# Performance work log

Measured on AMD Instinct MI355X. Metric: run time of the kernel, lower is better.

Reference implementation:

```python
import jax, jax.numpy as jnp
import numpy as np
from jax import lax

PRE_NMS_TOPN = 6000
POST_NMS_TOPN = 300
NMS_IOU = 0.7
VARIANCES = np.array([0.1, 0.1, 0.2, 0.2], dtype=np.float32)


def setup_inputs() -> dict:
    key = jax.random.key(0)
    k1, k2, k3, k4 = jax.random.split(key, 4)
    B, FH, FW, K = 32, 128, 128, 9
    A = FH * FW * K  # 147456 total anchors
    rpn_bbox_deltas = jax.random.normal(k1, (B, A, 4), dtype=jnp.float32) * 0.1
    rpn_labels = jax.random.normal(k2, (B, FH, FW, K), dtype=jnp.float32)
    # Anchors in [y1, x1, y2, x2] with y1<y2, x1<x2 on a ~1024px image.
    ctr = jax.random.uniform(k3, (A, 2), dtype=jnp.float32) * 1024.0
    wh = jax.random.uniform(k4, (A, 2), dtype=jnp.float32) * 224.0 + 32.0
    anchors = jnp.concatenate([ctr - 0.5 * wh, ctr + 0.5 * wh], axis=-1)
    return {"rpn_bbox_deltas": rpn_bbox_deltas, "rpn_labels": rpn_labels, "anchors": anchors}


def get_bboxes_from_deltas(anchors, deltas):
    # anchors: [A, 4] (y1,x1,y2,x2); deltas: [B, A, 4] (dy,dx,dh,dw)
    anc_w = anchors[..., 3] - anchors[..., 1]
    anc_h = anchors[..., 2] - anchors[..., 0]
    anc_cx = anchors[..., 1] + 0.5 * anc_w
    anc_cy = anchors[..., 0] + 0.5 * anc_h
    bb_w = jnp.exp(deltas[..., 3]) * anc_w
    bb_h = jnp.exp(deltas[..., 2]) * anc_h
    bb_cx = deltas[..., 1] * anc_w + anc_cx
    bb_cy = deltas[..., 0] * anc_h + anc_cy
    y1 = bb_cy - 0.5 * bb_h
    x1 = bb_cx - 0.5 * bb_w
    y2 = bb_h + y1
    x2 = bb_w + x1
    return jnp.stack([y1, x1, y2, x2], axis=-1)


def nms_per_image(boxes, scores, iou_threshold, num_keep):
    # boxes: [N, 4] sorted by descending score; scores: [N]
    y1, x1, y2, x2 = boxes[:, 0], boxes[:, 1], boxes[:, 2], boxes[:, 3]
    areas = (y2 - y1) * (x2 - x1)

    def step(scores_rem, _):
        idx = jnp.argmax(scores_rem)
        valid = jnp.isfinite(scores_rem[idx])
        b = boxes[idx]
        iy1 = jnp.maximum(b[0], y1)
        ix1 = jnp.maximum(b[1], x1)
        iy2 = jnp.minimum(b[2], y2)
        ix2 = jnp.minimum(b[3], x2)
        inter = jnp.clip(iy2 - iy1, 0.0) * jnp.clip(ix2 - ix1, 0.0)
        b_area = (b[2] - b[0]) * (b[3] - b[1])
        iou = inter / (areas + b_area - inter + 1e-9)
        # IoU(box, itself) == 1 > threshold, so the picked box is also suppressed.
        new_scores = jnp.where(iou > iou_threshold, -jnp.inf, scores_rem)
        return new_scores, (idx, valid)

    _, (keep_idx, valid) = lax.scan(step, scores, None, length=num_keep)
    vf = valid.astype(boxes.dtype)
    keep_boxes = boxes[keep_idx] * vf[:, None]  # zero-pad invalid slots
    keep_scores = scores[keep_idx] * vf
    return keep_boxes, keep_scores


def reference(rpn_bbox_deltas, rpn_labels, anchors):
    A = anchors.shape[0]
    B = rpn_bbox_deltas.shape[0]
    deltas = rpn_bbox_deltas.reshape(B, A, 4) * jnp.asarray(VARIANCES)
    labels = jax.nn.softmax(rpn_labels, axis=-1).reshape(B, A)
    rpn_bboxes = get_bboxes_from_deltas(anchors, deltas)  # [B, A, 4]
    # top-k pre-NMS filter (lax.top_k output is already sorted descending)
    pre_scores, pre_idx = lax.top_k(labels, PRE_NMS_TOPN)  # [B, P]
    pre_boxes = jnp.take_along_axis(rpn_bboxes, pre_idx[..., None], axis=1)  # [B, P, 4]
    nms_fn = lambda b, s: nms_per_image(b, s, NMS_IOU, POST_NMS_TOPN)
    roi_bboxes, roi_scores = jax.vmap(nms_fn)(pre_boxes, pre_scores)
    return roi_bboxes, roi_scores
```

## Files before the change

kernel.cpp:

```cpp
#include <hip/hip_runtime.h>
#include <cstdint>
#include <cstddef>

#pragma clang fp contract(off)

#define KCLS 9
#define PRE_N 6000
#define POST_N 300
#define NMS_IOU_T 0.7f
#define HIST_BLOCK 256
#define CHUNKS_PER_IMG 32
#define NMS_BLOCK 512
#define PICK_BLOCK 256
#define NSEG 8
#define SEG_CAP 2048
#define RANK_LDS 8192

#define SUPP(pb, pa, mbx, mar, out) \
    bool out; { \
        float iy1_ = fmaxf((pb).x, (mbx).x); \
        float ix1_ = fmaxf((pb).y, (mbx).y); \
        float iy2_ = fminf((pb).z, (mbx).z); \
        float ix2_ = fminf((pb).w, (mbx).w); \
        float ih_ = iy2_ - iy1_; ih_ = ih_ > 0.f ? ih_ : 0.f; \
        float iw_ = ix2_ - ix1_; iw_ = iw_ > 0.f ? iw_ : 0.f; \
        float inter_ = ih_ * iw_; \
        float den_ = (mar) + (pa) - inter_ + 1e-9f; \
        float hi_ = 0.7000007f * den_; \
        float lo_ = 0.6999993f * den_; \
        out = inter_ > hi_; \
        if (inter_ >= lo_ && inter_ <= hi_) out = (inter_ / den_) > NMS_IOU_T; \
    }

__global__ void __launch_bounds__(256)
softmax_hist_kernel(const float* __restrict__ labels,
                    float* __restrict__ scores,
                    unsigned int* __restrict__ ghist,
                    int gpi) {
    __shared__ float buf[256 * KCLS];
    __shared__ unsigned int h[2048];
    const int tid = threadIdx.x;
    for (int i = tid; i < 2048; i += 256) h[i] = 0u;

    const size_t gbase = (size_t)blockIdx.x * (256 * KCLS);
    const float4* lin4 = (const float4*)(labels + gbase);
    float4* b4 = (float4*)buf;
    for (int i = tid; i < 576; i += 256) b4[i] = lin4[i];
    __syncthreads();

    float v[KCLS];
    float m = -1e30f;
    #pragma unroll
    for (int k = 0; k < KCLS; ++k) { v[k] = buf[tid * KCLS + k]; m = fmaxf(m, v[k]); }
    float e[KCLS];
    float s = 0.f;
    #pragma unroll
    for (int k = 0; k < KCLS; ++k) { e[k] = expf(v[k] - m); s += e[k]; }
    #pragma unroll
    for (int k = 0; k < KCLS; ++k) {
        float r = e[k] / s;
        buf[tid * KCLS + k] = r;
        atomicAdd(&h[(__float_as_uint(r) >> 21) & 2047u], 1u);
    }
    __syncthreads();

    float4* o4 = (float4*)(scores + gbase);
    for (int i = tid; i < 576; i += 256) o4[i] = b4[i];

    const int img0 = (blockIdx.x * 256) / gpi;
    unsigned int* gh = ghist + (size_t)img0 * 2048;
    for (int i = tid; i < 2048; i += 256) {
        unsigned int c = h[i];
        if (c) atomicAdd(&gh[i], c);
    }
}

__global__ void hist_kernel(const float* __restrict__ scores,
                            unsigned int* __restrict__ ghist,
                            const unsigned int* __restrict__ state,
                            int A, int shift, int bins, unsigned int pmask) {
    __shared__ unsigned int h[2048];
    const int img = blockIdx.y;
    const int chunk = blockIdx.x;
    const int tid = threadIdx.x;
    for (int i = tid; i < bins; i += HIST_BLOCK) h[i] = 0u;
    __syncthreads();
    unsigned int prefix = state[img * 2 + 0] & pmask;
    const int per = A / CHUNKS_PER_IMG;
    const float* sc = scores + (size_t)img * A + (size_t)chunk * per;
    for (int i = tid; i < per; i += HIST_BLOCK) {
        unsigned int v = __float_as_uint(sc[i]);
        if ((v & pmask) == prefix)
            atomicAdd(&h[(v >> shift) & (unsigned)(bins - 1)], 1u);
    }
    __syncthreads();
    unsigned int* gh = ghist + (size_t)img * 2048;
    for (int i = tid; i < bins; i += HIST_BLOCK) {
        unsigned int c = h[i];
        if (c) atomicAdd(&gh[i], c);
    }
}

__global__ void __launch_bounds__(PICK_BLOCK)
pick_kernel(const unsigned int* __restrict__ ghist,
            unsigned int* __restrict__ state,
            int shift, int bins, int first_pass) {
    const int img = blockIdx.x;
    const int t = threadIdx.x;
    const unsigned int* gh = ghist + (size_t)img * 2048;
    __shared__ unsigned int cnt[2048];
    __shared__ unsigned int ssum[PICK_BLOCK];
    const int per = bins / PICK_BLOCK;
    unsigned int my = 0;
    for (int i = 0; i < per; ++i) {
        unsigned int c = gh[t * per + i];
        cnt[t * per + i] = c;
        my += c;
    }
    ssum[t] = my;
    __syncthreads();
    for (int d = 1; d < PICK_BLOCK; d <<= 1) {
        unsigned int v = (t + d < PICK_BLOCK) ? ssum[t + d] : 0u;
        __syncthreads();
        ssum[t] += v;
        __syncthreads();
    }
    unsigned int prefix = first_pass ? 0u : state[img * 2 + 0];
    unsigned int krem = first_pass ? (unsigned)PRE_N : state[img * 2 + 1];
    unsigned int above = ssum[t] - my;
    if (above < krem && ssum[t] >= krem) {
        unsigned int cum = above;
        for (int b = per - 1; b >= 0; --b) {
            unsigned int c = cnt[t * per + b];
            if (cum + c >= krem) {
                state[img * 2 + 0] = prefix | ((unsigned int)(t * per + b) << shift);
                state[img * 2 + 1] = krem - cum;
                break;
            }
            cum += c;
        }
    }
}

#define CE(a, b, u) { if ((v[a] > v[b]) == (u)) { unsigned long long t_ = v[a]; v[a] = v[b]; v[b] = t_; } }
#define REG3(u) { CE(0,4,u) CE(1,5,u) CE(2,6,u) CE(3,7,u) \
                  CE(0,2,u) CE(1,3,u) CE(4,6,u) CE(5,7,u) \
                  CE(0,1,u) CE(2,3,u) CE(4,5,u) CE(6,7,u) }

__global__ void __launch_bounds__(512)
compact_sort_kernel(const float* __restrict__ scores,
                    const unsigned int* __restrict__ state,
                    unsigned long long* __restrict__ pool,
                    unsigned int* __restrict__ counts,
                    int A) {
    __shared__ unsigned long long lin[SEG_CAP];
    __shared__ unsigned int plo[2][SEG_CAP];
    __shared__ unsigned int phi[2][SEG_CAP];
    __shared__ unsigned int cnt;
    const int img = blockIdx.y;
    const int seg = blockIdx.x;
    const int tid = threadIdx.x;
    const int lane = tid & 63;
    const int w = tid >> 6;
    const float* sc = scores + (size_t)img * A;
    const unsigned int T = state[img * 2 + 0];

    if (tid == 0) cnt = 0u;
    for (int i = tid; i < SEG_CAP; i += 512) lin[i] = ~0ull;
    __syncthreads();

    const int ngr = A >> 6;
    const int nj = ngr / NSEG;
    for (int j = w; j < nj; j += 8) {
        int g = seg + j * NSEG;
        int i = (g << 6) + lane;
        unsigned int sv = __float_as_uint(sc[i]);
        bool push = (sv >= T);
        unsigned long long bal = __ballot(push ? 1 : 0);
        if (push) {
            int leader = __ffsll(bal) - 1;
            int rank = __popcll(bal & ((1ull << lane) - 1ull));
            unsigned int base = 0;
            if (lane == leader) base = atomicAdd(&cnt, (unsigned int)__popcll(bal));
            base = (unsigned int)__shfl((int)base, leader);
            unsigned int pos = base + (unsigned int)rank;
            if (pos < SEG_CAP)
                lin[pos] = (((unsigned long long)(~sv)) << 32) | (unsigned long long)(unsigned int)i;
        }
    }
    __syncthreads();

    int n = (int)cnt; if (n > SEG_CAP) n = SEG_CAP;
    int P2 = 512; while (P2 < n) P2 <<= 1;
    const int NT = P2 >> 3;
    const int t = tid;
    const bool act = (t < NT);

    unsigned long long v[8];
    if (act) {
        #pragma unroll
        for (int e = 0; e < 8; ++e) v[e] = lin[(t << 3) + e];
        CE(0,1,true) CE(2,3,false) CE(4,5,true) CE(6,7,false)
        CE(0,2,true) CE(1,3,true) CE(4,6,false) CE(5,7,false)
        CE(0,1,true) CE(2,3,true) CE(4,5,false) CE(6,7,false)
        bool u8 = ((t & 1) == 0);
        REG3(u8)
    }
    int b = 0;
    for (int k = 16; k <= P2; k <<= 1) {
        const bool up = (((t << 3) & k) == 0);
        for (int j = k >> 1; j >= 8; j >>= 1) {
            const int c = j >> 3;
            if (act) {
                #pragma unroll
                for (int e = 0; e < 8; ++e) {
                    int idx = e * NT + t;
                    plo[b][idx] = (unsigned int)v[e];
                    phi[b][idx] = (unsigned int)(v[e] >> 32);
                }
            }
            __syncthreads();
            if (act) {
                const int q = t ^ c;
                const bool keep_min = (up == ((t & c) == 0));
                #pragma unroll
                for (int e = 0; e < 8; ++e) {
                    int idx = e * NT + q;
                    unsigned long long wv = ((unsigned long long)phi[b][idx] << 32)
                                          | (unsigned long long)plo[b][idx];
                    bool less = v[e] < wv;
                    v[e] = (less == keep_min) ? v[e] : wv;
                }
            }
            b ^= 1;
        }
        if (act) { REG3(up) }
    }

    unsigned long long* gp = pool + ((size_t)img * NSEG + seg) * SEG_CAP;
    if (act) {
        #pragma unroll
        for (int e = 0; e < 8; ++e) {
            int r = (t << 3) + e;
            if (r < n) gp[r] = v[e];
        }
    }
    if (tid == 0) counts[img * NSEG + seg] = (unsigned int)n;
}

__global__ void __launch_bounds__(256)
rank_decode_kernel(const unsigned long long* __restrict__ pool,
                   const unsigned int* __restrict__ counts,
                   const float* __restrict__ deltas,
                   const float* __restrict__ anchors,
                   float* __restrict__ pre_boxes,
                   float* __restrict__ pre_scores,
                   int A) {
    __shared__ unsigned long long arr[RANK_LDS];
    const int img = blockIdx.y;
    const int seg = blockIdx.x;
    const int tid = threadIdx.x;

    int c[NSEG], off[NSEG + 1];
    const unsigned long long* gp[NSEG];
    off[0] = 0;
    #pragma unroll
    for (int s = 0; s < NSEG; ++s) {
        int cs = (int)counts[img * NSEG + s];
        if (cs > SEG_CAP) cs = SEG_CAP;
        c[s] = cs;
        off[s + 1] = off[s] + cs;
        gp[s] = pool + ((size_t)img * NSEG + s) * SEG_CAP;
    }
    const int total = off[NSEG];
    const bool inlds = (total <= RANK_LDS);
    if (inlds) {
        #pragma unroll
        for (int s = 0; s < NSEG; ++s)
            for (int i = tid; i < c[s]; i += 256) arr[off[s] + i] = gp[s][i];
    }
    __syncthreads();

    const int m = c[seg];
    for (int i = tid; i < m; i += 256) {
        unsigned long long key = inlds ? arr[off[seg] + i] : gp[seg][i];
        int pos = i;
        #pragma unroll
        for (int s = 0; s < NSEG; ++s) {
            if (s == seg) continue;
            const unsigned long long* base = inlds ? (arr + off[s]) : gp[s];
            int lo = 0, hi = c[s];
            while (lo < hi) {
                int mid = (lo + hi) >> 1;
                if (base[mid] < key) lo = mid + 1; else hi = mid;
            }
            pos += lo;
        }
        if (pos < PRE_N) {
            unsigned int bidx = (unsigned int)(key & 0xFFFFFFFFull);
            unsigned int sbits = ~((unsigned int)(key >> 32));
            float score = __uint_as_float(sbits);
            float a0 = anchors[(size_t)bidx * 4 + 0];
            float a1 = anchors[(size_t)bidx * 4 + 1];
            float a2 = anchors[(size_t)bidx * 4 + 2];
            float a3 = anchors[(size_t)bidx * 4 + 3];
            const float* dd = deltas + ((size_t)img * A + bidx) * 4;
            float d0 = dd[0] * 0.1f;
            float d1 = dd[1] * 0.1f;
            float d2 = dd[2] * 0.2f;
            float d3 = dd[3] * 0.2f;
            float anc_w = a3 - a1;
            float anc_h = a2 - a0;
            float anc_cx = a1 + 0.5f * anc_w;
            float anc_cy = a0 + 0.5f * anc_h;
            float bb_w = expf(d3) * anc_w;
            float bb_h = expf(d2) * anc_h;
            float bb_cx = d1 * anc_w + anc_cx;
            float bb_cy = d0 * anc_h + anc_cy;
            float y1 = bb_cy - 0.5f * bb_h;
            float x1 = bb_cx - 0.5f * bb_w;
            float y2 = bb_h + y1;
            float x2 = bb_w + x1;
            float* ob = pre_boxes + ((size_t)img * PRE_N + pos) * 4;
            ob[0] = y1; ob[1] = x1; ob[2] = y2; ob[3] = x2;
            pre_scores[(size_t)img * PRE_N + pos] = score;
        }
    }
}

__global__ void __launch_bounds__(NMS_BLOCK)
nms_kernel(const float* __restrict__ pre_boxes,
           const float* __restrict__ pre_scores,
           float* __restrict__ out_boxes,
           float* __restrict__ out_scores) {
    const int img = blockIdx.x;
    const int tid = threadIdx.x;
    const int lane = tid & 63;
    const int grp = tid >> 6;
    const float4* bb4 = (const float4*)(pre_boxes + (size_t)img * PRE_N * 4);

    __shared__ float4 kept[POST_N];
    __shared__ float  kept_area[POST_N];
    __shared__ int    kept_idx[POST_N];
    __shared__ float4 chunkbox[64];
    __shared__ unsigned long long part[8][64];
    __shared__ unsigned long long supcol[64];
    __shared__ unsigned long long chunk_alive;
    __shared__ int kept_cnt;

    if (tid == 0) kept_cnt = 0;

    const int NCH = (PRE_N + 63) >> 6;

    float4 nb = make_float4(0.f, 0.f, 0.f, 0.f);
    if (grp == 0) nb = bb4[lane];

    for (int c = 0; c < NCH; ++c) {
        const int base = c << 6;
        if (grp == 0) chunkbox[lane] = nb;
        if (tid == 0) {
            int rem = PRE_N - base;
            chunk_alive = (rem >= 64) ? ~0ull : ((1ull << rem) - 1ull);
        }
        __syncthreads();

        if (grp == 0 && c + 1 < NCH) {
            int j = base + 64 + lane;
            nb = (j < PRE_N) ? bb4[j] : make_float4(0.f, 0.f, 0.f, 0.f);
        }

        const int K = kept_cnt;
        float4 mb = chunkbox[lane];
        float marea = (mb.z - mb.x) * (mb.w - mb.y);

        bool sup = false;
        for (int k = grp; k < K; k += 8) {
            float4 pb = kept[k];
            float pa = kept_area[k];
            SUPP(pb, pa, mb, marea, s)
            if (s) { sup = true; break; }
        }
        unsigned long long bal = __ballot(sup ? 1 : 0);
        if (lane == 0 && bal) atomicAnd(&chunk_alive, ~bal);

        unsigned long long pm = 0ull;
        #pragma unroll
        for (int u = 0; u < 8; ++u) {
            const int i = (grp << 3) + u;
            float4 pb = chunkbox[i];
            float pa = (pb.z - pb.x) * (pb.w - pb.y);
            SUPP(pb, pa, mb, marea, s)
            if (s) pm |= (1ull << i);
        }
        part[grp][lane] = pm;
        __syncthreads();

        if (grp == 0) {
            unsigned long long col = part[0][lane] | part[1][lane] | part[2][lane] | part[3][lane]
                                   | part[4][lane] | part[5][lane] | part[6][lane] | part[7][lane];
            supcol[lane] = col;
            const unsigned long long extm = chunk_alive;
            unsigned long long aliveset = 0ull;
            int kc = K;
            #pragma unroll 8
            for (int i = 0; i < 64; ++i) {
                unsigned long long mi = supcol[i];
                bool keep = (((extm >> i) & 1ull) != 0ull) &&
                            ((mi & aliveset) == 0ull) && (kc < POST_N);
                if (keep) {
                    if (lane == i) {
                        kept[kc] = mb;
                        kept_area[kc] = marea;
                        kept_idx[kc] = base + i;
                    }
                    aliveset |= (1ull << i);
                    ++kc;
                }
            }
            if (lane == 0) kept_cnt = kc;
        }
        __syncthreads();
        if (kept_cnt >= POST_N) break;
    }

    const int kc = kept_cnt;
    for (int r = tid; r < kc; r += NMS_BLOCK) {
        float4 bx = kept[r];
        float* ob = out_boxes + ((size_t)img * POST_N + r) * 4;
        ob[0] = bx.x; ob[1] = bx.y; ob[2] = bx.z; ob[3] = bx.w;
        out_scores[(size_t)img * POST_N + r] =
            pre_scores[(size_t)img * PRE_N + kept_idx[r]];
    }
}

extern "C" void kernel_launch(void* const* d_in, const int* in_sizes, int n_in,
                              void* d_out, int out_size, void* d_ws, size_t ws_size,
                              hipStream_t stream) {
    const float* deltas  = (const float*)d_in[0];
    const float* labels  = (const float*)d_in[1];
    const float* anchors = (const float*)d_in[2];
    float* out = (float*)d_out;

    const int A = in_sizes[2] / 4;
    const int B = in_sizes[0] / (A * 4);
    const int ngroups = in_sizes[1] / KCLS;
    const int gpi = ngroups / B;

    float* scores     = (float*)d_ws;
    float* pre_boxes  = scores + (size_t)B * A;
    float* pre_scores = pre_boxes + (size_t)B * PRE_N * 4;
    unsigned int* hist  = (unsigned int*)(pre_scores + (size_t)B * PRE_N);
    unsigned int* state = hist + (size_t)2 * B * 2048;
    unsigned long long* pool = (unsigned long long*)(state + (size_t)B * 2);
    unsigned int* counts = (unsigned int*)(pool + (size_t)B * NSEG * SEG_CAP);

    float* out_boxes  = out;
    float* out_scores = out + (size_t)B * POST_N * 4;

    hipMemsetAsync(d_out, 0, (size_t)out_size * sizeof(float), stream);
    hipMemsetAsync(hist, 0, ((size_t)2 * B * 2048 + 2 * B) * sizeof(unsigned int), stream);

    softmax_hist_kernel<<<ngroups / 256, 256, 0, stream>>>(
        labels, scores, hist + (size_t)0 * B * 2048, gpi);
    pick_kernel<<<B, PICK_BLOCK, 0, stream>>>(hist + (size_t)0 * B * 2048, state, 21, 2048, 1);

    dim3 hgrid(CHUNKS_PER_IMG, B);
    hist_kernel<<<hgrid, HIST_BLOCK, 0, stream>>>(
        scores, hist + (size_t)1 * B * 2048, state, A, 10, 2048, 0xFFE00000u);
    pick_kernel<<<B, PICK_BLOCK, 0, stream>>>(hist + (size_t)1 * B * 2048, state, 10, 2048, 0);

    dim3 sgrid(NSEG, B);
    compact_sort_kernel<<<sgrid, 512, 0, stream>>>(scores, state, pool, counts, A);
    rank_decode_kernel<<<sgrid, 256, 0, stream>>>(pool, counts, deltas, anchors,
                                                  pre_boxes, pre_scores, A);

    nms_kernel<<<B, NMS_BLOCK, 0, stream>>>(pre_boxes, pre_scores, out_boxes, out_scores);
}
```

Before: 260.9 us.

## Process 128-box chunks in NMS with 1024 threads and bitmask-driven serial pick

The NMS kernel now takes 128 candidate boxes per iteration with 1024 threads, where each of the 16 waves covers one half-chunk and one slot of the kept-box stride. Intra-chunk suppression rows are built with ballots into lo/hi bitmasks. The serial keep loop walks alive bits with ffs and shuffles instead of scanning all 64 entries. The next chunk is double-buffered in LDS so it can be written before the barrier. The aim is to halve the number of block-wide barrier rounds and shorten the serial resolve step, at the cost of more wasted IoU work once the kept list saturates mid-chunk.

```diff
diff --git a/kernel.cpp b/kernel.cpp
--- a/kernel.cpp
+++ b/kernel.cpp
@@ -10,11 +10,11 @@
 #define NMS_IOU_T 0.7f
 #define HIST_BLOCK 256
 #define CHUNKS_PER_IMG 32
-#define NMS_BLOCK 512
 #define PICK_BLOCK 256
 #define NSEG 8
 #define SEG_CAP 2048
 #define RANK_LDS 8192
+#define CHUNK2 128
 
 #define SUPP(pb, pa, mbx, mar, out) \
     bool out; { \
@@ -328,7 +328,7 @@
     }
 }
 
-__global__ void __launch_bounds__(NMS_BLOCK)
+__global__ void __launch_bounds__(1024)
 nms_kernel(const float* __restrict__ pre_boxes,
            const float* __restrict__ pre_scores,
            float* __restrict__ out_boxes,
@@ -337,85 +337,102 @@
     const int tid = threadIdx.x;
     const int lane = tid & 63;
     const int grp = tid >> 6;
+    const int half = grp & 1;
+    const int kslot = grp >> 1;
     const float4* bb4 = (const float4*)(pre_boxes + (size_t)img * PRE_N * 4);
 
     __shared__ float4 kept[POST_N];
     __shared__ float  kept_area[POST_N];
     __shared__ int    kept_idx[POST_N];
-    __shared__ float4 chunkbox[64];
-    __shared__ unsigned long long part[8][64];
-    __shared__ unsigned long long supcol[64];
-    __shared__ unsigned long long chunk_alive;
+    __shared__ float4 chunkbox[2][CHUNK2];
+    __shared__ unsigned long long rows_lo[CHUNK2];
+    __shared__ unsigned long long rows_hi[CHUNK2];
+    __shared__ unsigned long long alive_lo[2], alive_hi[2];
     __shared__ int kept_cnt;
 
-    if (tid == 0) kept_cnt = 0;
-
-    const int NCH = (PRE_N + 63) >> 6;
+    const int NPAIR = (PRE_N + CHUNK2 - 1) / CHUNK2;
 
     float4 nb = make_float4(0.f, 0.f, 0.f, 0.f);
-    if (grp == 0) nb = bb4[lane];
-
-    for (int c = 0; c < NCH; ++c) {
-        const int base = c << 6;
-        if (grp == 0) chunkbox[lane] = nb;
-        if (tid == 0) {
-            int rem = PRE_N - base;
-            chunk_alive = (rem >= 64) ? ~0ull : ((1ull << rem) - 1ull);
-        }
-        __syncthreads();
-
-        if (grp == 0 && c + 1 < NCH) {
-            int j = base + 64 + lane;
-            nb = (j < PRE_N) ? bb4[j] : make_float4(0.f, 0.f, 0.f, 0.f);
-        }
-
+    if (tid < CHUNK2) {
+        chunkbox[0][tid] = bb4[tid];
+        int j = CHUNK2 + tid;
+        nb = (j < PRE_N) ? bb4[j] : make_float4(0.f, 0.f, 0.f, 0.f);
+    }
+    if (tid == 0) { alive_lo[0] = ~0ull; alive_hi[0] = ~0ull; kept_cnt = 0; }
+    __syncthreads();
+
+    for (int p = 0; p < NPAIR; ++p) {
+        const int base = p * CHUNK2;
+        const int cur = p & 1;
         const int K = kept_cnt;
-        float4 mb = chunkbox[lane];
+        const int mybox = (half << 6) + lane;
+        float4 mb = chunkbox[cur][mybox];
         float marea = (mb.z - mb.x) * (mb.w - mb.y);
 
         bool sup = false;
-        for (int k = grp; k < K; k += 8) {
+        for (int k = kslot; k < K; k += 8) {
             float4 pb = kept[k];
             float pa = kept_area[k];
             SUPP(pb, pa, mb, marea, s)
             if (s) { sup = true; break; }
         }
         unsigned long long bal = __ballot(sup ? 1 : 0);
-        if (lane == 0 && bal) atomicAnd(&chunk_alive, ~bal);
-
-        unsigned long long pm = 0ull;
-        #pragma unroll
-        for (int u = 0; u < 8; ++u) {
-            const int i = (grp << 3) + u;
-            float4 pb = chunkbox[i];
+        if (lane == 0 && bal) {
+            if (half == 0) atomicAnd(&alive_lo[cur], ~bal);
+            else           atomicAnd(&alive_hi[cur], ~bal);
+        }
+
+        #pragma unroll 4
+        for (int u = 0; u < 16; ++u) {
+            const int i = (kslot << 4) + u;
+            float4 pb = chunkbox[cur][i];
             float pa = (pb.z - pb.x) * (pb.w - pb.y);
             SUPP(pb, pa, mb, marea, s)
-            if (s) pm |= (1ull << i);
-        }
-        part[grp][lane] = pm;
+            unsigned long long rb = __ballot(s ? 1 : 0);
+            if (lane == 0) {
+                if (half == 0) rows_lo[i] = rb; else rows_hi[i] = rb;
+            }
+        }
+
+        if (tid < CHUNK2) {
+            chunkbox[cur ^ 1][tid] = nb;
+            int j = base + 2 * CHUNK2 + tid;
+            nb = (j < PRE_N) ? bb4[j] : make_float4(0.f, 0.f, 0.f, 0.f);
+        }
+        if (tid == 0) {
+            int rem = PRE_N - (base + CHUNK2);
+            if (rem > 0) {
+                alive_lo[cur ^ 1] = (rem >= 64) ? ~0ull : ((1ull << rem) - 1ull);
+                int rh = rem - 64;
+                alive_hi[cur ^ 1] = (rh >= 64) ? ~0ull : ((rh > 0) ? ((1ull << rh) - 1ull) : 0ull);
+            }
+        }
         __syncthreads();
 
         if (grp == 0) {
-            unsigned long long col = part[0][lane] | part[1][lane] | part[2][lane] | part[3][lane]
-                                   | part[4][lane] | part[5][lane] | part[6][lane] | part[7][lane];
-            supcol[lane] = col;
-            const unsigned long long extm = chunk_alive;
-            unsigned long long aliveset = 0ull;
+            unsigned long long myA_lo = rows_lo[lane];
+            unsigned long long myA_hi = rows_hi[lane];
+            unsigned long long myB_lo = rows_lo[64 + lane];
+            unsigned long long myB_hi = rows_hi[64 + lane];
+            unsigned long long rlo = alive_lo[cur];
+            unsigned long long rhi = alive_hi[cur];
             int kc = K;
-            #pragma unroll 8
-            for (int i = 0; i < 64; ++i) {
-                unsigned long long mi = supcol[i];
-                bool keep = (((extm >> i) & 1ull) != 0ull) &&
-                            ((mi & aliveset) == 0ull) && (kc < POST_N);
-                if (keep) {
-                    if (lane == i) {
-                        kept[kc] = mb;
-                        kept_area[kc] = marea;
-                        kept_idx[kc] = base + i;
-                    }
-                    aliveset |= (1ull << i);
-                    ++kc;
+            while ((rlo | rhi) && kc < POST_N) {
+                const bool lo = (rlo != 0ull);
+                const int i = lo ? (__ffsll(rlo) - 1) : (64 + __ffsll(rhi) - 1);
+                if (lane == 0) {
+                    float4 kb = chunkbox[cur][i];
+                    kept[kc] = kb;
+                    kept_area[kc] = (kb.z - kb.x) * (kb.w - kb.y);
+                    kept_idx[kc] = base + i;
                 }
+                const int src = i & 63;
+                unsigned long long r_lo = __shfl(lo ? myA_lo : myB_lo, src);
+                unsigned long long r_hi = __shfl(lo ? myA_hi : myB_hi, src);
+                if (lo) rlo &= ~(1ull << i); else rhi &= ~(1ull << (i - 64));
+                rlo &= ~r_lo;
+                rhi &= ~r_hi;
+                ++kc;
             }
             if (lane == 0) kept_cnt = kc;
         }
@@ -424,7 +441,7 @@
     }
 
     const int kc = kept_cnt;
-    for (int r = tid; r < kc; r += NMS_BLOCK) {
+    for (int r = tid; r < kc; r += 1024) {
         float4 bx = kept[r];
         float* ob = out_boxes + ((size_t)img * POST_N + r) * 4;
         ob[0] = bx.x; ob[1] = bx.y; ob[2] = bx.z; ob[3] = bx.w;
@@ -474,5 +491,5 @@
     rank_decode_kernel<<<sgrid, 256, 0, stream>>>(pool, counts, deltas, anchors,
                                                   pre_boxes, pre_scores, A);
 
-    nms_kernel<<<B, NMS_BLOCK, 0, stream>>>(pre_boxes, pre_scores, out_boxes, out_scores);
-}
+    nms_kernel<<<B, 1024, 0, stream>>>(pre_boxes, pre_scores, out_boxes, out_scores);
+}
```

After: 301.8 us. +15.7%, slower.

## Double-buffer NMS chunk boxes and resolve intra-chunk keeps with ffs-driven row masks

Applied to the files above, without the earlier changes.

Chunk boxes are now double-buffered in shared memory and the next chunk is prefetched inside the same phase, which removes one __syncthreads per chunk. Intra-chunk suppression is built as per-row ballot masks instead of per-thread column masks OR-reduced across groups. The serial keep loop now walks only surviving candidates with find-first-set and shuffles each kept row's mask, instead of testing all 64 slots. This shortens the serial per-chunk critical path, at the cost of more ballots in the pairwise stage.

```diff
diff --git a/kernel.cpp b/kernel.cpp
--- a/kernel.cpp
+++ b/kernel.cpp
@@ -342,35 +342,26 @@
     __shared__ float4 kept[POST_N];
     __shared__ float  kept_area[POST_N];
     __shared__ int    kept_idx[POST_N];
-    __shared__ float4 chunkbox[64];
-    __shared__ unsigned long long part[8][64];
-    __shared__ unsigned long long supcol[64];
-    __shared__ unsigned long long chunk_alive;
+    __shared__ float4 chunkbox[2][64];
+    __shared__ unsigned long long rows[64];
+    __shared__ unsigned long long supball[8];
     __shared__ int kept_cnt;
 
+    const int NCH = (PRE_N + 63) >> 6;
+
+    float4 nb = make_float4(0.f, 0.f, 0.f, 0.f);
+    if (tid < 64) {
+        chunkbox[0][tid] = bb4[tid];
+        nb = bb4[64 + tid];
+    }
     if (tid == 0) kept_cnt = 0;
-
-    const int NCH = (PRE_N + 63) >> 6;
-
-    float4 nb = make_float4(0.f, 0.f, 0.f, 0.f);
-    if (grp == 0) nb = bb4[lane];
+    __syncthreads();
 
     for (int c = 0; c < NCH; ++c) {
         const int base = c << 6;
-        if (grp == 0) chunkbox[lane] = nb;
-        if (tid == 0) {
-            int rem = PRE_N - base;
-            chunk_alive = (rem >= 64) ? ~0ull : ((1ull << rem) - 1ull);
-        }
-        __syncthreads();
-
-        if (grp == 0 && c + 1 < NCH) {
-            int j = base + 64 + lane;
-            nb = (j < PRE_N) ? bb4[j] : make_float4(0.f, 0.f, 0.f, 0.f);
-        }
-
+        const int cur = c & 1;
         const int K = kept_cnt;
-        float4 mb = chunkbox[lane];
+        float4 mb = chunkbox[cur][lane];
         float marea = (mb.z - mb.x) * (mb.w - mb.y);
 
         bool sup = false;
@@ -381,41 +372,44 @@
             if (s) { sup = true; break; }
         }
         unsigned long long bal = __ballot(sup ? 1 : 0);
-        if (lane == 0 && bal) atomicAnd(&chunk_alive, ~bal);
-
-        unsigned long long pm = 0ull;
+        if (lane == 0) supball[grp] = bal;
+
         #pragma unroll
         for (int u = 0; u < 8; ++u) {
             const int i = (grp << 3) + u;
-            float4 pb = chunkbox[i];
+            float4 pb = chunkbox[cur][i];
             float pa = (pb.z - pb.x) * (pb.w - pb.y);
             SUPP(pb, pa, mb, marea, s)
-            if (s) pm |= (1ull << i);
-        }
-        part[grp][lane] = pm;
+            unsigned long long rb = __ballot(s ? 1 : 0);
+            if (lane == 0) rows[i] = rb;
+        }
+
+        if (tid < 64) {
+            chunkbox[cur ^ 1][tid] = nb;
+            int j = base + 128 + tid;
+            nb = (j < PRE_N) ? bb4[j] : make_float4(0.f, 0.f, 0.f, 0.f);
+        }
         __syncthreads();
 
         if (grp == 0) {
-            unsigned long long col = part[0][lane] | part[1][lane] | part[2][lane] | part[3][lane]
-                                   | part[4][lane] | part[5][lane] | part[6][lane] | part[7][lane];
-            supcol[lane] = col;
-            const unsigned long long extm = chunk_alive;
-            unsigned long long aliveset = 0ull;
+            const int remn = PRE_N - base;
+            unsigned long long ext = (remn >= 64) ? ~0ull : ((1ull << remn) - 1ull);
+            unsigned long long sb = supball[0] | supball[1] | supball[2] | supball[3]
+                                  | supball[4] | supball[5] | supball[6] | supball[7];
+            unsigned long long rem = ext & ~sb;
+            unsigned long long myrow = rows[lane];
             int kc = K;
-            #pragma unroll 8
-            for (int i = 0; i < 64; ++i) {
-                unsigned long long mi = supcol[i];
-                bool keep = (((extm >> i) & 1ull) != 0ull) &&
-                            ((mi & aliveset) == 0ull) && (kc < POST_N);
-                if (keep) {
-                    if (lane == i) {
-                        kept[kc] = mb;
-                        kept_area[kc] = marea;
-                        kept_idx[kc] = base + i;
-                    }
-                    aliveset |= (1ull << i);
-                    ++kc;
+            while (rem && kc < POST_N) {
+                const int i = __ffsll(rem) - 1;
+                if (lane == i) {
+                    kept[kc] = mb;
+                    kept_area[kc] = marea;
+                    kept_idx[kc] = base + i;
                 }
+                unsigned long long ri = __shfl(myrow, i);
+                rem &= ~(1ull << i);
+                rem &= ~ri;
+                ++kc;
             }
             if (lane == 0) kept_cnt = kc;
         }
```

Measured after the change: 261.9 us. No clear change (+0.4%).
